# Kernel optimization log

Hardware: AMD Instinct MI355X
Metric: run time of the kernel (lower is better)

Reference implementation:

```python
import jax, jax.numpy as jnp
import numpy as np

N = 100000
E = 1600000
IN_C = 256
HID = 128
OUT_C = 128
HEADS = 4
C_HEAD = HID // HEADS
BN_EPS = 1e-5
NEG_SLOPE = 0.2


def setup_inputs() -> dict:
    key = jax.random.key(0)
    ks = jax.random.split(key, 12)
    s = lambda fan: 1.0 / np.sqrt(fan)
    return {
        "x": jax.random.normal(ks[0], (N, IN_C), dtype=jnp.float32),
        "W_gat": jax.random.normal(ks[1], (IN_C, HID), dtype=jnp.float32) * s(IN_C),
        "att_src": jax.random.normal(ks[2], (HEADS, C_HEAD), dtype=jnp.float32) * s(C_HEAD),
        "att_dst": jax.random.normal(ks[3], (HEADS, C_HEAD), dtype=jnp.float32) * s(C_HEAD),
        "bias_gat": jnp.zeros((HID,), dtype=jnp.float32),
        "bn1_gamma": jnp.ones((HID,), dtype=jnp.float32),
        "bn1_beta": jnp.zeros((HID,), dtype=jnp.float32),
        "eps_gin": jnp.zeros((), dtype=jnp.float32),
        "lin_W": jax.random.normal(ks[4], (HID, OUT_C), dtype=jnp.float32) * s(HID),
        "lin_b": jnp.zeros((OUT_C,), dtype=jnp.float32),
        "bn2_gamma": jnp.ones((OUT_C,), dtype=jnp.float32),
        "bn2_beta": jnp.zeros((OUT_C,), dtype=jnp.float32),
        "edge_index": jax.random.randint(ks[5], (2, E), 0, N, dtype=jnp.int64),
    }


def batch_norm(h, gamma, beta):
    mu = jnp.mean(h, axis=0)
    var = jnp.var(h, axis=0)
    return (h - mu) * jax.lax.rsqrt(var + BN_EPS) * gamma + beta


def reference(x, W_gat, att_src, att_dst, bias_gat, bn1_gamma, bn1_beta,
              eps_gin, lin_W, lin_b, bn2_gamma, bn2_beta, edge_index):
    src, dst = edge_index[0], edge_index[1]
    # ---- GATConv ----
    h = (x @ W_gat).reshape(N, HEADS, C_HEAD)              # [N,H,C]
    a_src = jnp.einsum('nhc,hc->nh', h, att_src)            # [N,H]
    a_dst = jnp.einsum('nhc,hc->nh', h, att_dst)            # [N,H]
    e = jax.nn.leaky_relu(a_src[src] + a_dst[dst], NEG_SLOPE)  # [E,H]
    # segment softmax over incoming edges of each dst node
    m = jax.ops.segment_max(e, dst, num_segments=N)         # [N,H]
    num = jnp.exp(e - m[dst])                                # [E,H]
    den = jax.ops.segment_sum(num, dst, num_segments=N)      # [N,H]
    alpha = num / den[dst]                                   # [E,H]
    msg = alpha[:, :, None] * h[src]                         # [E,H,C]
    out1 = jax.ops.segment_sum(msg, dst, num_segments=N)     # [N,H,C]
    out1 = out1.reshape(N, HID) + bias_gat
    # BN + ELU (dropout = identity in eval)
    out1 = jax.nn.elu(batch_norm(out1, bn1_gamma, bn1_beta))
    # ---- GINConv: nn((1+eps)*x + sum_neighbors) ----
    agg = jax.ops.segment_sum(out1[src], dst, num_segments=N)
    z = (1.0 + eps_gin) * out1 + agg
    out2 = z @ lin_W + lin_b
    out2 = jax.nn.elu(batch_norm(out2, bn2_gamma, bn2_beta))
    return out2
```

## Files before the change

kernel.cpp:

```cpp
#include <hip/hip_runtime.h>

#define N_NODES 100000
#define N_EDGES 1600000
#define IN_C 256
#define HID 128
#define NEG_SLOPE 0.2f
#define BN_EPS 1e-5f
#define NBUCK 391
#define NPART 391

typedef unsigned int uint32;
typedef __attribute__((ext_vector_type(8))) short bf16x8;
typedef __attribute__((ext_vector_type(4))) float f32x4;

__device__ __forceinline__ float lrelu(float x) { return x > 0.f ? x : NEG_SLOPE * x; }

__device__ __forceinline__ unsigned short f2bf(float f) {
    uint32 u = __float_as_uint(f);
    u += 0x7fffu + ((u >> 16) & 1u);
    return (unsigned short)(u >> 16);
}
__device__ __forceinline__ float bf2f(unsigned short h) {
    return __uint_as_float(((uint32)h) << 16);
}
__device__ __forceinline__ float bflo(uint32 v) { return __uint_as_float(v << 16); }
__device__ __forceinline__ float bfhi(uint32 v) { return __uint_as_float(v & 0xffff0000u); }
__device__ __forceinline__ uint32 packbf(float a, float b) {
    return (uint32)f2bf(a) | ((uint32)f2bf(b) << 16);
}

__global__ void k_init(int* __restrict__ bcount, float* __restrict__ bnacc) {
    int t = threadIdx.x;
    if (t < NBUCK) bcount[t] = 0;
    if (t < 512) bnacc[t] = 0.f;
}

__global__ void k_transpose_all(const float* __restrict__ W1, const float* __restrict__ W2,
                                unsigned short* __restrict__ Wt1,
                                unsigned short* __restrict__ Wt2) {
    int idx = blockIdx.x * 256 + threadIdx.x;
    if (idx < IN_C * 128) {
        int k = idx >> 7, n = idx & 127;
        Wt1[n * IN_C + k] = f2bf(W1[idx]);
    } else {
        idx -= IN_C * 128;
        if (idx < HID * 128) {
            int k = idx >> 7, n = idx & 127;
            Wt2[n * HID + k] = f2bf(W2[idx]);
        }
    }
}

template <bool AF32, bool OUTF32>
__global__ __launch_bounds__(256) void k_gemm(const void* __restrict__ Av,
                                              const unsigned short* __restrict__ Wt,
                                              void* __restrict__ Out, int K) {
    __shared__ unsigned short As[128 * 72];
    __shared__ unsigned short Bs[128 * 72];
    const int t = threadIdx.x;
    const int n0 = blockIdx.x * 128;
    const int wv = t >> 6, lane = t & 63;
    const int wy = wv >> 1, wx = wv & 1;
    const int lm = lane & 15, lg = lane >> 4;
    const float* Af = (const float*)Av;
    const unsigned short* Ah = (const unsigned short*)Av;

    f32x4 acc[4][4];
#pragma unroll
    for (int i = 0; i < 4; ++i)
#pragma unroll
        for (int j = 0; j < 4; ++j) acc[i][j] = (f32x4){0.f, 0.f, 0.f, 0.f};

    float4 afp[8];
    uint4 ahp[4];
    uint4 bvp[4];

    if (AF32) {
#pragma unroll
        for (int p = 0; p < 8; ++p) {
            int idx = p * 256 + t, row = idx >> 4, c4 = idx & 15, gn = n0 + row;
            afp[p] = (gn < N_NODES) ? *(const float4*)&Af[(size_t)gn * K + c4 * 4]
                                    : make_float4(0.f, 0.f, 0.f, 0.f);
        }
    } else {
#pragma unroll
        for (int p = 0; p < 4; ++p) {
            int idx = p * 256 + t, row = idx >> 3, c = idx & 7, gn = n0 + row;
            ahp[p] = (gn < N_NODES) ? *(const uint4*)&Ah[(size_t)gn * K + c * 8]
                                    : make_uint4(0, 0, 0, 0);
        }
    }
#pragma unroll
    for (int p = 0; p < 4; ++p) {
        int idx = p * 256 + t, n = idx >> 3, c = idx & 7;
        bvp[p] = *(const uint4*)&Wt[(size_t)n * K + c * 8];
    }

    for (int kc = 0; kc < K; kc += 64) {
        if (AF32) {
#pragma unroll
            for (int p = 0; p < 8; ++p) {
                int idx = p * 256 + t, row = idx >> 4, c4 = idx & 15;
                ushort4 b;
                b.x = f2bf(afp[p].x); b.y = f2bf(afp[p].y);
                b.z = f2bf(afp[p].z); b.w = f2bf(afp[p].w);
                *(ushort4*)&As[row * 72 + c4 * 4] = b;
            }
        } else {
#pragma unroll
            for (int p = 0; p < 4; ++p) {
                int idx = p * 256 + t, row = idx >> 3, c = idx & 7;
                *(uint4*)&As[row * 72 + c * 8] = ahp[p];
            }
        }
#pragma unroll
        for (int p = 0; p < 4; ++p) {
            int idx = p * 256 + t, n = idx >> 3, c = idx & 7;
            *(uint4*)&Bs[n * 72 + c * 8] = bvp[p];
        }
        __syncthreads();
        int kn = kc + 64;
        if (kn < K) {
            if (AF32) {
#pragma unroll
                for (int p = 0; p < 8; ++p) {
                    int idx = p * 256 + t, row = idx >> 4, c4 = idx & 15, gn = n0 + row;
                    afp[p] = (gn < N_NODES) ? *(const float4*)&Af[(size_t)gn * K + kn + c4 * 4]
                                            : make_float4(0.f, 0.f, 0.f, 0.f);
                }
            } else {
#pragma unroll
                for (int p = 0; p < 4; ++p) {
                    int idx = p * 256 + t, row = idx >> 3, c = idx & 7, gn = n0 + row;
                    ahp[p] = (gn < N_NODES) ? *(const uint4*)&Ah[(size_t)gn * K + kn + c * 8]
                                            : make_uint4(0, 0, 0, 0);
                }
            }
#pragma unroll
            for (int p = 0; p < 4; ++p) {
                int idx = p * 256 + t, n = idx >> 3, c = idx & 7;
                bvp[p] = *(const uint4*)&Wt[(size_t)n * K + kn + c * 8];
            }
        }
#pragma unroll
        for (int ks = 0; ks < 2; ++ks) {
            bf16x8 af[4], bfr[4];
#pragma unroll
            for (int i = 0; i < 4; ++i)
                af[i] = *(const bf16x8*)&As[(wy * 64 + i * 16 + lm) * 72 + ks * 32 + lg * 8];
#pragma unroll
            for (int j = 0; j < 4; ++j)
                bfr[j] = *(const bf16x8*)&Bs[(wx * 64 + j * 16 + lm) * 72 + ks * 32 + lg * 8];
#pragma unroll
            for (int i = 0; i < 4; ++i)
#pragma unroll
                for (int j = 0; j < 4; ++j)
                    acc[i][j] = __builtin_amdgcn_mfma_f32_16x16x32_bf16(af[i], bfr[j],
                                                                        acc[i][j], 0, 0, 0);
        }
        __syncthreads();
    }
#pragma unroll
    for (int i = 0; i < 4; ++i) {
#pragma unroll
        for (int r = 0; r < 4; ++r) {
            int row = n0 + wy * 64 + i * 16 + lg * 4 + r;
            if (row < N_NODES) {
#pragma unroll
                for (int j = 0; j < 4; ++j) {
                    int col = wx * 64 + j * 16 + lm;
                    float v = acc[i][j][r];
                    if (OUTF32) ((float*)Out)[(size_t)row * 128 + col] = v;
                    else ((unsigned short*)Out)[(size_t)row * 128 + col] = f2bf(v);
                }
            }
        }
    }
}

__global__ __launch_bounds__(256) void k_att(const unsigned short* __restrict__ hb,
                                             const float* __restrict__ att_s,
                                             const float* __restrict__ att_d,
                                             float* __restrict__ a_src,
                                             float* __restrict__ a_dst) {
    int node = blockIdx.x * 2 + (threadIdx.x >> 7);
    int c = threadIdx.x & 127;
    float hv = bf2f(hb[(size_t)node * 128 + c]);
    float ps = hv * att_s[c];
    float pd = hv * att_d[c];
#pragma unroll
    for (int m = 1; m < 32; m <<= 1) {
        ps += __shfl_xor(ps, m);
        pd += __shfl_xor(pd, m);
    }
    if ((c & 31) == 0) {
        int head = c >> 5;
        a_src[node * 4 + head] = ps;
        a_dst[node * 4 + head] = pd;
    }
}

__global__ __launch_bounds__(256) void k_bucket_count(const int* __restrict__ ei,
                                                      int* __restrict__ bcount) {
    __shared__ int hist[NBUCK];
    for (int i = threadIdx.x; i < NBUCK; i += 256) hist[i] = 0;
    __syncthreads();
    for (int e = blockIdx.x * 256 + threadIdx.x; e < N_EDGES; e += gridDim.x * 256)
        atomicAdd(&hist[ei[N_EDGES + e] >> 8], 1);
    __syncthreads();
    for (int i = threadIdx.x; i < NBUCK; i += 256)
        if (hist[i]) atomicAdd(&bcount[i], hist[i]);
}

__global__ void k_bucket_scan(const int* __restrict__ bcount, int* __restrict__ bucket_base,
                              int* __restrict__ gcursor, int* __restrict__ row_ptr) {
    __shared__ int sh[512];
    int t = threadIdx.x;
    int v0 = (t < NBUCK) ? bcount[t] : 0;
    int val = v0;
    sh[t] = val;
    __syncthreads();
    for (int off = 1; off < 512; off <<= 1) {
        int o = (t >= off) ? sh[t - off] : 0;
        __syncthreads();
        val += o;
        sh[t] = val;
        __syncthreads();
    }
    if (t < NBUCK) {
        int e = val - v0;
        bucket_base[t] = e;
        gcursor[t] = e;
    }
    if (t == 0) {
        bucket_base[NBUCK] = N_EDGES;
        row_ptr[N_NODES] = N_EDGES;
    }
}

__global__ __launch_bounds__(256) void k_partition(const int* __restrict__ ei,
                                                   int* __restrict__ gcursor,
                                                   int* __restrict__ staging) {
    __shared__ int hist[NBUCK];
    __shared__ int base[NBUCK];
    int t = threadIdx.x;
    int e0 = blockIdx.x * 4096;
    for (int i = t; i < NBUCK; i += 256) hist[i] = 0;
    __syncthreads();
    int pk[16], cb[16];
#pragma unroll
    for (int u = 0; u < 16; ++u) {
        int e = e0 + u * 256 + t;
        cb[u] = -1;
        if (e < N_EDGES) {
            int s = ei[e], d = ei[N_EDGES + e];
            int b = d >> 8;
            int r = atomicAdd(&hist[b], 1);
            pk[u] = ((d & 255) << 17) | s;
            cb[u] = (r << 9) | b;
        }
    }
    __syncthreads();
    for (int i = t; i < NBUCK; i += 256)
        if (hist[i]) base[i] = atomicAdd(&gcursor[i], hist[i]);
    __syncthreads();
#pragma unroll
    for (int u = 0; u < 16; ++u) {
        if (cb[u] >= 0) {
            int b = cb[u] & 511, r = cb[u] >> 9;
            staging[base[b] + r] = pk[u];
        }
    }
}

__global__ __launch_bounds__(256) void k_bucket_sort(const int* __restrict__ staging,
                                                     const int* __restrict__ bucket_base,
                                                     int* __restrict__ row_ptr,
                                                     int* __restrict__ sorted_src) {
    __shared__ int hist[256];
    __shared__ int sh[256];
    int t = threadIdx.x, b = blockIdx.x;
    int lo = bucket_base[b], hi = bucket_base[b + 1];
    hist[t] = 0;
    __syncthreads();
    for (int i = lo + t; i < hi; i += 256) atomicAdd(&hist[staging[i] >> 17], 1);
    __syncthreads();
    int v0 = hist[t];
    int val = v0;
    sh[t] = val;
    __syncthreads();
    for (int off = 1; off < 256; off <<= 1) {
        int o = (t >= off) ? sh[t - off] : 0;
        __syncthreads();
        val += o;
        sh[t] = val;
        __syncthreads();
    }
    int excl = val - v0;
    int d = b * 256 + t;
    if (d < N_NODES) row_ptr[d] = lo + excl;
    hist[t] = excl;
    __syncthreads();
    for (int i = lo + t; i < hi; i += 256) {
        int p = staging[i];
        int r = atomicAdd(&hist[p >> 17], 1);
        sorted_src[lo + r] = p & 0x1FFFF;
    }
}

__global__ __launch_bounds__(256) void k_gat_agg(const uint4* __restrict__ h4,
                                                 const float* __restrict__ a_src,
                                                 const float* __restrict__ a_dst,
                                                 const int* __restrict__ row_ptr,
                                                 const int* __restrict__ sorted_src,
                                                 uint4* __restrict__ out1b4) {
    __shared__ int sbuf[4][64];
    __shared__ float wbuf[4][64][4];
    int lane = threadIdx.x & 63, wv = threadIdx.x >> 6;
    int sub = lane >> 4, chl = lane & 15, hd = chl >> 2;
    int node = blockIdx.x * 4 + wv;
    int start = row_ptr[node];
    int deg = row_ptr[node + 1] - start;
    if (deg == 0) {
        if (lane < 16) out1b4[((uint32)node << 4) + chl] = make_uint4(0u, 0u, 0u, 0u);
        return;
    }
    float4 ad = *(const float4*)&a_dst[node * 4];
    float4 den4 = make_float4(0.f, 0.f, 0.f, 0.f);
    float acc[8] = {0.f, 0.f, 0.f, 0.f, 0.f, 0.f, 0.f, 0.f};
    for (int j0 = 0; j0 < deg; j0 += 64) {
        int j = j0 + lane;
        int s = 0;
        float4 w = make_float4(0.f, 0.f, 0.f, 0.f);
        if (j < deg) {
            s = sorted_src[start + j];
            float4 as = *(const float4*)&a_src[s * 4];
            w.x = __expf(lrelu(as.x + ad.x));
            w.y = __expf(lrelu(as.y + ad.y));
            w.z = __expf(lrelu(as.z + ad.z));
            w.w = __expf(lrelu(as.w + ad.w));
        }
        den4.x += w.x; den4.y += w.y; den4.z += w.z; den4.w += w.w;
        sbuf[wv][lane] = s;
        *(float4*)&wbuf[wv][lane][0] = w;
        __builtin_amdgcn_wave_barrier();
        int nj16 = (min(64, deg - j0) + 15) & ~15;
        for (int jj = 0; jj < nj16; jj += 16) {
#pragma unroll
            for (int u = 0; u < 4; ++u) {
                int e = jj + u * 4 + sub;
                int ss = sbuf[wv][e];
                float wh = wbuf[wv][e][hd];
                uint4 hv = h4[((uint32)ss << 4) + chl];
                acc[0] += wh * bflo(hv.x); acc[1] += wh * bfhi(hv.x);
                acc[2] += wh * bflo(hv.y); acc[3] += wh * bfhi(hv.y);
                acc[4] += wh * bflo(hv.z); acc[5] += wh * bfhi(hv.z);
                acc[6] += wh * bflo(hv.w); acc[7] += wh * bfhi(hv.w);
            }
        }
        __builtin_amdgcn_wave_barrier();
    }
#pragma unroll
    for (int m = 16; m < 64; m <<= 1)
#pragma unroll
        for (int c = 0; c < 8; ++c) acc[c] += __shfl_xor(acc[c], m);
#pragma unroll
    for (int m = 1; m < 64; m <<= 1) {
        den4.x += __shfl_xor(den4.x, m);
        den4.y += __shfl_xor(den4.y, m);
        den4.z += __shfl_xor(den4.z, m);
        den4.w += __shfl_xor(den4.w, m);
    }
    float den = hd == 0 ? den4.x : hd == 1 ? den4.y : hd == 2 ? den4.z : den4.w;
    float rden = 1.f / den;
    if (lane < 16) {
        uint4 o;
        o.x = packbf(acc[0] * rden, acc[1] * rden);
        o.y = packbf(acc[2] * rden, acc[3] * rden);
        o.z = packbf(acc[4] * rden, acc[5] * rden);
        o.w = packbf(acc[6] * rden, acc[7] * rden);
        out1b4[((uint32)node << 4) + chl] = o;
    }
}

__global__ __launch_bounds__(256) void k_gin_agg(const uint4* __restrict__ ob4,
                                                 const int* __restrict__ row_ptr,
                                                 const int* __restrict__ sorted_src,
                                                 const float* __restrict__ eps_ptr,
                                                 uint4* __restrict__ zb4) {
    __shared__ int sbuf[4][64];
    __shared__ float mbuf[4][64];
    int lane = threadIdx.x & 63, wv = threadIdx.x >> 6;
    int sub = lane >> 4, chl = lane & 15;
    int node = blockIdx.x * 4 + wv;
    int start = row_ptr[node];
    int deg = row_ptr[node + 1] - start;
    float acc[8] = {0.f, 0.f, 0.f, 0.f, 0.f, 0.f, 0.f, 0.f};
    for (int j0 = 0; j0 < deg; j0 += 64) {
        int j = j0 + lane;
        int s = 0;
        float m = 0.f;
        if (j < deg) { s = sorted_src[start + j]; m = 1.f; }
        sbuf[wv][lane] = s;
        mbuf[wv][lane] = m;
        __builtin_amdgcn_wave_barrier();
        int nj16 = (min(64, deg - j0) + 15) & ~15;
        for (int jj = 0; jj < nj16; jj += 16) {
#pragma unroll
            for (int u = 0; u < 4; ++u) {
                int e = jj + u * 4 + sub;
                int ss = sbuf[wv][e];
                float mm = mbuf[wv][e];
                uint4 hv = ob4[((uint32)ss << 4) + chl];
                acc[0] += mm * bflo(hv.x); acc[1] += mm * bfhi(hv.x);
                acc[2] += mm * bflo(hv.y); acc[3] += mm * bfhi(hv.y);
                acc[4] += mm * bflo(hv.z); acc[5] += mm * bfhi(hv.z);
                acc[6] += mm * bflo(hv.w); acc[7] += mm * bfhi(hv.w);
            }
        }
        __builtin_amdgcn_wave_barrier();
    }
#pragma unroll
    for (int m = 16; m < 64; m <<= 1)
#pragma unroll
        for (int c = 0; c < 8; ++c) acc[c] += __shfl_xor(acc[c], m);
    if (lane < 16) {
        float ep = 1.f + eps_ptr[0];
        uint4 own = ob4[((uint32)node << 4) + chl];
        uint4 o;
        o.x = packbf(fmaf(ep, bflo(own.x), acc[0]), fmaf(ep, bfhi(own.x), acc[1]));
        o.y = packbf(fmaf(ep, bflo(own.y), acc[2]), fmaf(ep, bfhi(own.y), acc[3]));
        o.z = packbf(fmaf(ep, bflo(own.z), acc[4]), fmaf(ep, bfhi(own.z), acc[5]));
        o.w = packbf(fmaf(ep, bflo(own.w), acc[6]), fmaf(ep, bfhi(own.w), acc[7]));
        zb4[((uint32)node << 4) + chl] = o;
    }
}

__global__ __launch_bounds__(256) void k_bnstats_bf16(const uint32* __restrict__ buf,
                                                      float* __restrict__ acc) {
    __shared__ float sh[4][64][4];
    int lane = threadIdx.x & 63, grp = threadIdx.x >> 6;
    float s0 = 0.f, s1 = 0.f, q0 = 0.f, q1 = 0.f;
    for (int r = blockIdx.x * 4 + grp; r < N_NODES; r += gridDim.x * 4) {
        uint32 v = buf[(size_t)r * 64 + lane];
        float v0 = bflo(v), v1 = bfhi(v);
        s0 += v0; s1 += v1; q0 += v0 * v0; q1 += v1 * v1;
    }
    sh[grp][lane][0] = s0; sh[grp][lane][1] = s1;
    sh[grp][lane][2] = q0; sh[grp][lane][3] = q1;
    __syncthreads();
    if (grp == 0) {
#pragma unroll
        for (int g = 1; g < 4; ++g) {
            s0 += sh[g][lane][0]; s1 += sh[g][lane][1];
            q0 += sh[g][lane][2]; q1 += sh[g][lane][3];
        }
        int c0 = lane * 2;
        atomicAdd(&acc[c0], s0);
        atomicAdd(&acc[c0 + 1], s1);
        atomicAdd(&acc[128 + c0], q0);
        atomicAdd(&acc[128 + c0 + 1], q1);
    }
}

__global__ __launch_bounds__(256) void k_bn_elu_b16(uint32* __restrict__ buf,
                                                    const float* __restrict__ acc,
                                                    const float* __restrict__ gamma,
                                                    const float* __restrict__ beta) {
    __shared__ float psc[128], psh[128];
    int t = threadIdx.x;
    if (t < 128) {
        float mu = acc[t] * (1.f / N_NODES);
        float var = acc[128 + t] * (1.f / N_NODES) - mu * mu;
        float s = rsqrtf(var + BN_EPS) * gamma[t];
        psc[t] = s;
        psh[t] = beta[t] - mu * s;
    }
    __syncthreads();
    size_t i = (size_t)blockIdx.x * 256 + t;
    if (i >= (size_t)N_NODES * 64) return;
    int c0 = (int)(i & 63) * 2;
    uint32 v = buf[i];
    float r0 = fmaf(bflo(v), psc[c0], psh[c0]);
    float r1 = fmaf(bfhi(v), psc[c0 + 1], psh[c0 + 1]);
    r0 = r0 > 0.f ? r0 : __expf(r0) - 1.f;
    r1 = r1 > 0.f ? r1 : __expf(r1) - 1.f;
    buf[i] = packbf(r0, r1);
}

__global__ __launch_bounds__(256) void k_bn_elu_out(const uint32* __restrict__ in,
                                                    const float* __restrict__ acc,
                                                    const float* __restrict__ gamma,
                                                    const float* __restrict__ beta,
                                                    float2* __restrict__ out) {
    __shared__ float psc[128], psh[128];
    int t = threadIdx.x;
    if (t < 128) {
        float mu = acc[t] * (1.f / N_NODES);
        float var = acc[128 + t] * (1.f / N_NODES) - mu * mu;
        float s = rsqrtf(var + BN_EPS) * gamma[t];
        psc[t] = s;
        psh[t] = beta[t] - mu * s;
    }
    __syncthreads();
    size_t i = (size_t)blockIdx.x * 256 + t;
    if (i >= (size_t)N_NODES * 64) return;
    int c0 = (int)(i & 63) * 2;
    uint32 v = in[i];
    float r0 = fmaf(bflo(v), psc[c0], psh[c0]);
    float r1 = fmaf(bfhi(v), psc[c0 + 1], psh[c0 + 1]);
    r0 = r0 > 0.f ? r0 : __expf(r0) - 1.f;
    r1 = r1 > 0.f ? r1 : __expf(r1) - 1.f;
    out[i] = make_float2(r0, r1);
}

extern "C" void kernel_launch(void* const* d_in, const int* in_sizes, int n_in,
                              void* d_out, int out_size, void* d_ws, size_t ws_size,
                              hipStream_t stream) {
    (void)in_sizes; (void)n_in; (void)out_size; (void)ws_size;
    const float* x       = (const float*)d_in[0];
    const float* W_gat   = (const float*)d_in[1];
    const float* att_src = (const float*)d_in[2];
    const float* att_dst = (const float*)d_in[3];
    const float* bn1_g   = (const float*)d_in[5];
    const float* bn1_b   = (const float*)d_in[6];
    const float* eps_gin = (const float*)d_in[7];
    const float* lin_W   = (const float*)d_in[8];
    const float* bn2_g   = (const float*)d_in[10];
    const float* bn2_b   = (const float*)d_in[11];
    const int*   ei      = (const int*)d_in[12];
    float* out = (float*)d_out;

    char* w = (char*)d_ws;
    size_t o = 0;
    auto take = [&](size_t b) -> char* {
        char* p = w + o;
        o += (b + 255) & ~(size_t)255;
        return p;
    };
    unsigned short* hb   = (unsigned short*)take((size_t)N_NODES * 128 * 2);
    unsigned short* Wt1  = (unsigned short*)take((size_t)128 * IN_C * 2);
    unsigned short* Wt2  = (unsigned short*)take((size_t)128 * HID * 2);
    uint32* o1b          = (uint32*)take((size_t)N_NODES * 64 * 4);
    float* a_src         = (float*)take((size_t)N_NODES * 4 * 4);
    float* a_dst         = (float*)take((size_t)N_NODES * 4 * 4);
    int*   sorted        = (int*)take((size_t)N_EDGES * 4);
    int*   staging       = (int*)take((size_t)N_EDGES * 4);
    int*   row_ptr       = (int*)take((size_t)(N_NODES + 1) * 4);
    int*   bcount        = (int*)take((NBUCK + 1) * 4);
    int*   bucket_base   = (int*)take((NBUCK + 1) * 4);
    int*   gcursor       = (int*)take((NBUCK + 1) * 4);
    float* bnacc         = (float*)take(512 * 4);
    uint32* zb  = (uint32*)hb;
    uint32* o2b = o1b;

    const int nGemmBlocks = (N_NODES + 127) / 128;
    const int nElemBlocks = (N_NODES * 64 + 255) / 256;

    k_init<<<1, 512, 0, stream>>>(bcount, bnacc);
    k_transpose_all<<<((IN_C + HID) * 128 + 255) / 256, 256, 0, stream>>>(W_gat, lin_W,
                                                                          Wt1, Wt2);
    k_gemm<true, false><<<nGemmBlocks, 256, 0, stream>>>(x, Wt1, hb, IN_C);
    k_att<<<N_NODES / 2, 256, 0, stream>>>(hb, att_src, att_dst, a_src, a_dst);
    k_bucket_count<<<256, 256, 0, stream>>>(ei, bcount);
    k_bucket_scan<<<1, 512, 0, stream>>>(bcount, bucket_base, gcursor, row_ptr);
    k_partition<<<NPART, 256, 0, stream>>>(ei, gcursor, staging);
    k_bucket_sort<<<NBUCK, 256, 0, stream>>>(staging, bucket_base, row_ptr, sorted);
    k_gat_agg<<<N_NODES / 4, 256, 0, stream>>>((const uint4*)hb, a_src, a_dst, row_ptr,
                                               sorted, (uint4*)o1b);
    k_bnstats_bf16<<<512, 256, 0, stream>>>(o1b, bnacc);
    k_bn_elu_b16<<<nElemBlocks, 256, 0, stream>>>(o1b, bnacc, bn1_g, bn1_b);
    k_gin_agg<<<N_NODES / 4, 256, 0, stream>>>((const uint4*)o1b, row_ptr, sorted,
                                               eps_gin, (uint4*)zb);
    k_gemm<false, false><<<nGemmBlocks, 256, 0, stream>>>(zb, Wt2, o2b, HID);
    k_bnstats_bf16<<<512, 256, 0, stream>>>(o2b, bnacc + 256);
    k_bn_elu_out<<<nElemBlocks, 256, 0, stream>>>(o2b, bnacc + 256, bn2_g, bn2_b,
                                                  (float2*)out);
}
```

Before: 542.0 us.

## Remap GAT/GIN aggregation to one edge per wave with per-lane channel pairs

Both neighbor-aggregation kernels change from 4 edges per pass, with 16 lanes each loading a uint4, to a whole wave reading one 256-byte source row per edge, one uint32 (two bf16 channels) per lane. Source indices are broadcast with readlane instead of going through shared memory. Eight independent row loads are batched per step, and each lane accumulates its own denominator, which removes the cross-lane shuffle reductions at the end. The trade-off is narrower per-lane loads and more serial edge iterations per wave, in exchange for fewer shuffles and less LDS traffic.

Result: no change. 546.3 us (+0.8%).

```diff
diff --git a/kernel.cpp b/kernel.cpp
--- a/kernel.cpp
+++ b/kernel.cpp
@@ -308,132 +308,112 @@
     }
 }
 
-__global__ __launch_bounds__(256) void k_gat_agg(const uint4* __restrict__ h4,
+__global__ __launch_bounds__(256) void k_gat_agg(const uint32* __restrict__ h32,
                                                  const float* __restrict__ a_src,
                                                  const float* __restrict__ a_dst,
                                                  const int* __restrict__ row_ptr,
                                                  const int* __restrict__ sorted_src,
-                                                 uint4* __restrict__ out1b4) {
-    __shared__ int sbuf[4][64];
-    __shared__ float wbuf[4][64][4];
+                                                 uint32* __restrict__ out1) {
+    __shared__ alignas(16) float wbuf[4][4][72];
     int lane = threadIdx.x & 63, wv = threadIdx.x >> 6;
-    int sub = lane >> 4, chl = lane & 15, hd = chl >> 2;
+    int hd = lane >> 4;
     int node = blockIdx.x * 4 + wv;
     int start = row_ptr[node];
     int deg = row_ptr[node + 1] - start;
     if (deg == 0) {
-        if (lane < 16) out1b4[((uint32)node << 4) + chl] = make_uint4(0u, 0u, 0u, 0u);
+        out1[((uint32)node << 6) + lane] = 0u;
         return;
     }
     float4 ad = *(const float4*)&a_dst[node * 4];
-    float4 den4 = make_float4(0.f, 0.f, 0.f, 0.f);
-    float acc[8] = {0.f, 0.f, 0.f, 0.f, 0.f, 0.f, 0.f, 0.f};
+    float acc0 = 0.f, acc1 = 0.f, den = 0.f;
     for (int j0 = 0; j0 < deg; j0 += 64) {
-        int j = j0 + lane;
+        int m = min(64, deg - j0);
         int s = 0;
         float4 w = make_float4(0.f, 0.f, 0.f, 0.f);
-        if (j < deg) {
-            s = sorted_src[start + j];
+        if (lane < m) {
+            s = sorted_src[start + j0 + lane];
             float4 as = *(const float4*)&a_src[s * 4];
             w.x = __expf(lrelu(as.x + ad.x));
             w.y = __expf(lrelu(as.y + ad.y));
             w.z = __expf(lrelu(as.z + ad.z));
             w.w = __expf(lrelu(as.w + ad.w));
         }
-        den4.x += w.x; den4.y += w.y; den4.z += w.z; den4.w += w.w;
-        sbuf[wv][lane] = s;
-        *(float4*)&wbuf[wv][lane][0] = w;
+        wbuf[wv][0][lane] = w.x;
+        wbuf[wv][1][lane] = w.y;
+        wbuf[wv][2][lane] = w.z;
+        wbuf[wv][3][lane] = w.w;
         __builtin_amdgcn_wave_barrier();
-        int nj16 = (min(64, deg - j0) + 15) & ~15;
-        for (int jj = 0; jj < nj16; jj += 16) {
-#pragma unroll
-            for (int u = 0; u < 4; ++u) {
-                int e = jj + u * 4 + sub;
-                int ss = sbuf[wv][e];
-                float wh = wbuf[wv][e][hd];
-                uint4 hv = h4[((uint32)ss << 4) + chl];
-                acc[0] += wh * bflo(hv.x); acc[1] += wh * bfhi(hv.x);
-                acc[2] += wh * bflo(hv.y); acc[3] += wh * bfhi(hv.y);
-                acc[4] += wh * bflo(hv.z); acc[5] += wh * bfhi(hv.z);
-                acc[6] += wh * bflo(hv.w); acc[7] += wh * bfhi(hv.w);
-            }
+        int e0 = 0;
+        for (; e0 + 8 <= m; e0 += 8) {
+            uint32 hr[8];
+#pragma unroll
+            for (int k = 0; k < 8; ++k) {
+                int ss = __builtin_amdgcn_readlane(s, e0 + k);
+                hr[k] = h32[((uint32)ss << 6) + lane];
+            }
+            float4 w0 = *(const float4*)&wbuf[wv][hd][e0];
+            float4 w1 = *(const float4*)&wbuf[wv][hd][e0 + 4];
+            float wk[8] = {w0.x, w0.y, w0.z, w0.w, w1.x, w1.y, w1.z, w1.w};
+#pragma unroll
+            for (int k = 0; k < 8; ++k) {
+                den += wk[k];
+                acc0 = fmaf(wk[k], bflo(hr[k]), acc0);
+                acc1 = fmaf(wk[k], bfhi(hr[k]), acc1);
+            }
+        }
+        for (; e0 < m; ++e0) {
+            int ss = __builtin_amdgcn_readlane(s, e0);
+            uint32 hv = h32[((uint32)ss << 6) + lane];
+            float wk = wbuf[wv][hd][e0];
+            den += wk;
+            acc0 = fmaf(wk, bflo(hv), acc0);
+            acc1 = fmaf(wk, bfhi(hv), acc1);
         }
         __builtin_amdgcn_wave_barrier();
     }
-#pragma unroll
-    for (int m = 16; m < 64; m <<= 1)
-#pragma unroll
-        for (int c = 0; c < 8; ++c) acc[c] += __shfl_xor(acc[c], m);
-#pragma unroll
-    for (int m = 1; m < 64; m <<= 1) {
-        den4.x += __shfl_xor(den4.x, m);
-        den4.y += __shfl_xor(den4.y, m);
-        den4.z += __shfl_xor(den4.z, m);
-        den4.w += __shfl_xor(den4.w, m);
-    }
-    float den = hd == 0 ? den4.x : hd == 1 ? den4.y : hd == 2 ? den4.z : den4.w;
     float rden = 1.f / den;
-    if (lane < 16) {
-        uint4 o;
-        o.x = packbf(acc[0] * rden, acc[1] * rden);
-        o.y = packbf(acc[2] * rden, acc[3] * rden);
-        o.z = packbf(acc[4] * rden, acc[5] * rden);
-        o.w = packbf(acc[6] * rden, acc[7] * rden);
-        out1b4[((uint32)node << 4) + chl] = o;
-    }
-}
-
-__global__ __launch_bounds__(256) void k_gin_agg(const uint4* __restrict__ ob4,
+    out1[((uint32)node << 6) + lane] = packbf(acc0 * rden, acc1 * rden);
+}
+
+__global__ __launch_bounds__(256) void k_gin_agg(const uint32* __restrict__ ob,
                                                  const int* __restrict__ row_ptr,
                                                  const int* __restrict__ sorted_src,
                                                  const float* __restrict__ eps_ptr,
-                                                 uint4* __restrict__ zb4) {
-    __shared__ int sbuf[4][64];
-    __shared__ float mbuf[4][64];
+                                                 uint32* __restrict__ zb) {
     int lane = threadIdx.x & 63, wv = threadIdx.x >> 6;
-    int sub = lane >> 4, chl = lane & 15;
     int node = blockIdx.x * 4 + wv;
     int start = row_ptr[node];
     int deg = row_ptr[node + 1] - start;
-    float acc[8] = {0.f, 0.f, 0.f, 0.f, 0.f, 0.f, 0.f, 0.f};
+    float acc0 = 0.f, acc1 = 0.f;
     for (int j0 = 0; j0 < deg; j0 += 64) {
-        int j = j0 + lane;
+        int m = min(64, deg - j0);
         int s = 0;
-        float m = 0.f;
-        if (j < deg) { s = sorted_src[start + j]; m = 1.f; }
-        sbuf[wv][lane] = s;
-        mbuf[wv][lane] = m;
-        __builtin_amdgcn_wave_barrier();
-        int nj16 = (min(64, deg - j0) + 15) & ~15;
-        for (int jj = 0; jj < nj16; jj += 16) {
-#pragma unroll
-            for (int u = 0; u < 4; ++u) {
-                int e = jj + u * 4 + sub;
-                int ss = sbuf[wv][e];
-                float mm = mbuf[wv][e];
-                uint4 hv = ob4[((uint32)ss << 4) + chl];
-                acc[0] += mm * bflo(hv.x); acc[1] += mm * bfhi(hv.x);
-                acc[2] += mm * bflo(hv.y); acc[3] += mm * bfhi(hv.y);
-                acc[4] += mm * bflo(hv.z); acc[5] += mm * bfhi(hv.z);
-                acc[6] += mm * bflo(hv.w); acc[7] += mm * bfhi(hv.w);
-            }
-        }
-        __builtin_amdgcn_wave_barrier();
-    }
-#pragma unroll
-    for (int m = 16; m < 64; m <<= 1)
-#pragma unroll
-        for (int c = 0; c < 8; ++c) acc[c] += __shfl_xor(acc[c], m);
-    if (lane < 16) {
-        float ep = 1.f + eps_ptr[0];
-        uint4 own = ob4[((uint32)node << 4) + chl];
-        uint4 o;
-        o.x = packbf(fmaf(ep, bflo(own.x), acc[0]), fmaf(ep, bfhi(own.x), acc[1]));
-        o.y = packbf(fmaf(ep, bflo(own.y), acc[2]), fmaf(ep, bfhi(own.y), acc[3]));
-        o.z = packbf(fmaf(ep, bflo(own.z), acc[4]), fmaf(ep, bfhi(own.z), acc[5]));
-        o.w = packbf(fmaf(ep, bflo(own.w), acc[6]), fmaf(ep, bfhi(own.w), acc[7]));
-        zb4[((uint32)node << 4) + chl] = o;
-    }
+        if (lane < m) s = sorted_src[start + j0 + lane];
+        int e0 = 0;
+        for (; e0 + 8 <= m; e0 += 8) {
+            uint32 hr[8];
+#pragma unroll
+            for (int k = 0; k < 8; ++k) {
+                int ss = __builtin_amdgcn_readlane(s, e0 + k);
+                hr[k] = ob[((uint32)ss << 6) + lane];
+            }
+#pragma unroll
+            for (int k = 0; k < 8; ++k) {
+                acc0 += bflo(hr[k]);
+                acc1 += bfhi(hr[k]);
+            }
+        }
+        for (; e0 < m; ++e0) {
+            int ss = __builtin_amdgcn_readlane(s, e0);
+            uint32 hv = ob[((uint32)ss << 6) + lane];
+            acc0 += bflo(hv);
+            acc1 += bfhi(hv);
+        }
+    }
+    float ep = 1.f + eps_ptr[0];
+    uint32 own = ob[((uint32)node << 6) + lane];
+    zb[((uint32)node << 6) + lane] = packbf(fmaf(ep, bflo(own), acc0),
+                                            fmaf(ep, bfhi(own), acc1));
 }
 
 __global__ __launch_bounds__(256) void k_bnstats_bf16(const uint32* __restrict__ buf,
@@ -566,12 +546,11 @@
     k_bucket_scan<<<1, 512, 0, stream>>>(bcount, bucket_base, gcursor, row_ptr);
     k_partition<<<NPART, 256, 0, stream>>>(ei, gcursor, staging);
     k_bucket_sort<<<NBUCK, 256, 0, stream>>>(staging, bucket_base, row_ptr, sorted);
-    k_gat_agg<<<N_NODES / 4, 256, 0, stream>>>((const uint4*)hb, a_src, a_dst, row_ptr,
-                                               sorted, (uint4*)o1b);
+    k_gat_agg<<<N_NODES / 4, 256, 0, stream>>>((const uint32*)hb, a_src, a_dst, row_ptr,
+                                               sorted, o1b);
     k_bnstats_bf16<<<512, 256, 0, stream>>>(o1b, bnacc);
     k_bn_elu_b16<<<nElemBlocks, 256, 0, stream>>>(o1b, bnacc, bn1_g, bn1_b);
-    k_gin_agg<<<N_NODES / 4, 256, 0, stream>>>((const uint4*)o1b, row_ptr, sorted,
-                                               eps_gin, (uint4*)zb);
+    k_gin_agg<<<N_NODES / 4, 256, 0, stream>>>(o1b, row_ptr, sorted, eps_gin, zb);
     k_gemm<false, false><<<nGemmBlocks, 256, 0, stream>>>(zb, Wt2, o2b, HID);
     k_bnstats_bf16<<<512, 256, 0, stream>>>(o2b, bnacc + 256);
     k_bn_elu_out<<<nElemBlocks, 256, 0, stream>>>(o2b, bnacc + 256, bn2_g, bn2_b,
```
